# Kernel optimization log

Measured on AMD Instinct MI355X. Metric: run time of the kernel, lower is better.

The kernel has to match this reference:

```python
import jax, jax.numpy as jnp
import numpy as np

BETA = 0.25  # commitment_beta


def setup_inputs() -> dict:
    key = jax.random.key(0)
    k1, k2 = jax.random.split(key)
    B, C, H, W = 8, 256, 32, 32
    n_embed = 16384
    x = jax.random.normal(k1, (B, C, H, W), dtype=jnp.float32)
    # torch init: uniform_(-1/codebook_size, 1/codebook_size)
    weight = jax.random.uniform(k2, (n_embed, C), dtype=jnp.float32,
                                minval=-1.0 / n_embed, maxval=1.0 / n_embed)
    return {"x": x, "weight": weight}


def reference(x, weight):
    B, C, H, W = x.shape
    # b c h w -> b (h w) c
    xf = jnp.transpose(x, (0, 2, 3, 1)).reshape(B, H * W, C)
    flat = xf.reshape(-1, C)  # [N, C], N = B*H*W
    d = (jnp.sum(flat * flat, axis=1, keepdims=True)
         + jnp.sum(weight * weight, axis=1)[None, :]
         - 2.0 * flat @ weight.T)
    idx = jnp.argmin(d, axis=-1)          # [N]
    xq = weight[idx].reshape(B, H * W, C)  # codebook gather
    sg = jax.lax.stop_gradient
    loss = (BETA * jnp.mean((sg(xq) - xf) ** 2)
            + jnp.mean((xq - sg(xf)) ** 2))
    # straight-through estimator
    xq_st = xf + sg(xq - xf)
    # b (h w) c -> b c h w
    xq_img = jnp.transpose(xq_st.reshape(B, H, W, C), (0, 3, 1, 2))
    x_code = idx.reshape(B, H, W)
    return xq_img, loss, x_code
```

## Files before the change

### kernel.cpp

```cpp
#include <hip/hip_runtime.h>
#include <stdint.h>

#define NROW    8192
#define CDIM    256
#define NCODE   16384
#define MARGINF 6.0e-5f

typedef short short8 __attribute__((ext_vector_type(8)));
typedef float floatx4 __attribute__((ext_vector_type(4)));
typedef _Float16 half2v __attribute__((ext_vector_type(2)));

__device__ inline ushort f2bf(float f) {
    unsigned u = __builtin_bit_cast(unsigned, f);
    unsigned r = (u + 0x7fffu + ((u >> 16) & 1u)) >> 16;
    return (ushort)r;
}
__device__ inline unsigned fsort(float v) {
    unsigned u = __builtin_bit_cast(unsigned, v);
    return (u >> 31) ? ~u : (u | 0x80000000u);
}

__device__ inline void gl_lds16(const ushort* g, ushort* lds) {
    __builtin_amdgcn_global_load_lds(
        (const __attribute__((address_space(1))) unsigned int*)(g),
        (__attribute__((address_space(3))) unsigned int*)(lds),
        16, 0, 0);
}

__global__ __launch_bounds__(256) void prep_x(const float* __restrict__ x,
                                              float* __restrict__ xf32,
                                              ushort* __restrict__ xbf) {
    __shared__ float tile[32][33];
    const int b = blockIdx.x, ht = blockIdx.y, ct = blockIdx.z;
    const int t = threadIdx.x;
    const int hw0 = ht * 32, c0 = ct * 32;
    {
        const int cc = t >> 5, hh = t & 31;
        #pragma unroll
        for (int i = 0; i < 4; ++i) {
            int cl = cc + i * 8;
            tile[cl][hh] = x[((size_t)(b * 256 + c0 + cl) << 10) + hw0 + hh];
        }
    }
    __syncthreads();
    {
        const int col = t & 31, row = t >> 5;
        #pragma unroll
        for (int i = 0; i < 4; ++i) {
            int r = row + i * 8;
            float v = tile[col][r];
            size_t o = ((size_t)(b * 1024 + hw0 + r) << 8) + c0 + col;
            xf32[o] = v;
            xbf[o] = f2bf(v);
        }
    }
}

__global__ __launch_bounds__(256) void prep_w2(const float* __restrict__ w,
                                               ushort* __restrict__ wbf,
                                               float* __restrict__ S2a) {
#pragma clang fp contract(off)
    const int gt = blockIdx.x * 256 + threadIdx.x;
    const int j = gt >> 1, h = gt & 1;
    const float* a = w + ((size_t)j << 8) + h * 128;
    ushort* orow = wbf + ((size_t)j << 8) + h * 128;
    float r8[8];
    #pragma unroll
    for (int l = 0; l < 8; ++l) { float v = a[l]; r8[l] = v * v; }
    for (int i = 8; i < 128; i += 8) {
        #pragma unroll
        for (int l = 0; l < 8; ++l) { float v = a[i + l]; r8[l] = r8[l] + v * v; }
    }
    float hs = ((r8[0] + r8[1]) + (r8[2] + r8[3])) + ((r8[4] + r8[5]) + (r8[6] + r8[7]));
    float other = __shfl_xor(hs, 1);
    if (h == 0) S2a[j] = hs + other;
    for (int i = 0; i < 128; i += 8) {
        ushort u8[8];
        #pragma unroll
        for (int l = 0; l < 8; ++l) u8[l] = f2bf(a[i + l]);
        *(ushort4*)(orow + i)     = make_ushort4(u8[0], u8[1], u8[2], u8[3]);
        *(ushort4*)(orow + i + 4) = make_ushort4(u8[4], u8[5], u8[6], u8[7]);
    }
}

__global__ __launch_bounds__(256) void gemm_min(const ushort* __restrict__ Wb,
                                                const ushort* __restrict__ Xb,
                                                const float* __restrict__ S2a,
                                                ushort* __restrict__ bm16) {
    __shared__ __attribute__((aligned(16))) ushort As[8192];
    __shared__ __attribute__((aligned(16))) ushort Bs[8192];
    __shared__ __attribute__((aligned(16))) ushort stg[128 * 8];

    const int n0 = blockIdx.x * 128;
    const int j0 = blockIdx.y * 128;
    const int t  = threadIdx.x;
    const int wv = t >> 6, l = t & 63;
    const int wr = wv >> 1, wc = wv & 1;
    const int q  = l >> 4, c = l & 15;

    const int lr = l >> 3;
    const int lperm = (l & 7) ^ lr;
    const size_t gA0 = ((size_t)(j0 + wv * 32 + lr) << 8) + lperm * 8;
    const size_t gB0 = ((size_t)(n0 + wv * 32 + lr) << 8) + lperm * 8;
    const int ldsbase = wv * 2048;

    floatx4 acc[4][4];
    #pragma unroll
    for (int mi = 0; mi < 4; ++mi)
        #pragma unroll
        for (int ni = 0; ni < 4; ++ni)
            acc[mi][ni] = (floatx4){0.f, 0.f, 0.f, 0.f};

    for (int kb = 0; kb < 4; ++kb) {
        if (kb) __syncthreads();
        #pragma unroll
        for (int ca = 0; ca < 4; ++ca) {
            gl_lds16(Wb + gA0 + ca * 2048 + kb * 64, As + ldsbase + ca * 512);
            gl_lds16(Xb + gB0 + ca * 2048 + kb * 64, Bs + ldsbase + ca * 512);
        }
        __syncthreads();
        #pragma unroll
        for (int kk = 0; kk < 2; ++kk) {
            short8 af[4], bf[4];
            #pragma unroll
            for (int mi = 0; mi < 4; ++mi) {
                int row = wr * 64 + mi * 16 + c;
                int pos = (kk * 4 + q) ^ (c & 7);
                af[mi] = *(const short8*)&As[row * 64 + pos * 8];
            }
            #pragma unroll
            for (int ni = 0; ni < 4; ++ni) {
                int row = wc * 64 + ni * 16 + c;
                int pos = (kk * 4 + q) ^ (c & 7);
                bf[ni] = *(const short8*)&Bs[row * 64 + pos * 8];
            }
            #pragma unroll
            for (int mi = 0; mi < 4; ++mi)
                #pragma unroll
                for (int ni = 0; ni < 4; ++ni)
                    acc[mi][ni] = __builtin_amdgcn_mfma_f32_16x16x32_bf16(
                        af[mi], bf[ni], acc[mi][ni], 0, 0, 0);
        }
    }

    #pragma unroll
    for (int mi = 0; mi < 4; ++mi) {
        float4 s2 = *(const float4*)&S2a[j0 + wr * 64 + mi * 16 + (q << 2)];
        #pragma unroll
        for (int ni = 0; ni < 4; ++ni) {
            float m0 = fmaf(-2.f, acc[mi][ni][0], s2.x);
            float m1 = fmaf(-2.f, acc[mi][ni][1], s2.y);
            float m2 = fmaf(-2.f, acc[mi][ni][2], s2.z);
            float m3 = fmaf(-2.f, acc[mi][ni][3], s2.w);
            float m = fminf(fminf(m0, m1), fminf(m2, m3));
            m = fminf(m, __shfl_xor(m, 16));
            m = fminf(m, __shfl_xor(m, 32));
            if (q == 0) {
                int qr = wc * 64 + ni * 16 + c;
                stg[qr * 8 + wr * 4 + mi] =
                    __builtin_bit_cast(ushort, (_Float16)m);
            }
        }
    }
    __syncthreads();
    if (t < 128) {
        uint4 v = *(const uint4*)&stg[t * 8];
        *(uint4*)(bm16 + ((size_t)(n0 + t) << 10) + blockIdx.y * 8) = v;
    }
}

__global__ __launch_bounds__(256) void rescore5(const ushort* __restrict__ bm16,
                                                const float* __restrict__ xf32,
                                                const float* __restrict__ w,
                                                const float* __restrict__ S2a,
                                                int* __restrict__ idxb,
                                                float* __restrict__ xcode,
                                                float* __restrict__ lpart) {
#pragma clang fp contract(off)
    __shared__ float xs[4][256];
    __shared__ short list[4][128];
    __shared__ int ncand[4];

    const int t = threadIdx.x, wv = t >> 6, l = t & 63;
    const int n = blockIdx.x * 4 + wv;
    if (l == 0) ncand[wv] = 0;

    const float4 xv = *(const float4*)&xf32[((size_t)n << 8) + l * 4];
    *(float4*)&xs[wv][l * 4] = xv;

    const uint4* bp = (const uint4*)(bm16 + ((size_t)n << 10) + l * 16);
    const uint4 b0 = bp[0], b1 = bp[1];
    float vals[16];
    {
        unsigned uu[8] = {b0.x, b0.y, b0.z, b0.w, b1.x, b1.y, b1.z, b1.w};
        #pragma unroll
        for (int i = 0; i < 8; ++i) {
            half2v h = __builtin_bit_cast(half2v, uu[i]);
            vals[2 * i]     = (float)h[0];
            vals[2 * i + 1] = (float)h[1];
        }
    }
    float vmin = vals[0];
    #pragma unroll
    for (int i = 1; i < 16; ++i) vmin = fminf(vmin, vals[i]);
    #pragma unroll
    for (int off = 1; off <= 32; off <<= 1) vmin = fminf(vmin, __shfl_xor(vmin, off));
    const float thr = vmin + MARGINF;
    #pragma unroll
    for (int i = 0; i < 16; ++i)
        if (vals[i] <= thr) {
            int p = atomicAdd(&ncand[wv], 1);
            if (p < 128) list[wv][p] = (short)(l * 16 + i);
        }

    float racc = 0.f;
    if (l < 16) {
        const float* a_ = &xs[wv][(l >> 3) * 128];
        const int ai = l & 7;
        float v = a_[ai];
        racc = v * v;
        for (int i = 8; i < 128; i += 8) { v = a_[i + ai]; racc = racc + v * v; }
    }
    racc = racc + __shfl_xor(racc, 1);
    racc = racc + __shfl_xor(racc, 2);
    racc = racc + __shfl_xor(racc, 4);
    racc = racc + __shfl_xor(racc, 8);
    const float S1n = __shfl(racc, 0);

    const int ntot = (ncand[wv] < 128 ? ncand[wv] : 128) * 16;
    unsigned long long best = ~0ull;
    for (int s = l; s < ntot; s += 64) {
        const int j = (int)list[wv][s >> 4] * 16 + (s & 15);
        const float4* wr4 = (const float4*)(w + ((size_t)j << 8));
        float g = 0.f;
        #pragma unroll
        for (int half = 0; half < 4; ++half) {
            float4 buf[16];
            #pragma unroll
            for (int i = 0; i < 16; ++i) buf[i] = wr4[half * 16 + i];
            #pragma unroll
            for (int i = 0; i < 16; ++i) {
                const float4 xv4 = *(const float4*)&xs[wv][half * 64 + i * 4];
                g = fmaf(xv4.x, buf[i].x, g);
                g = fmaf(xv4.y, buf[i].y, g);
                g = fmaf(xv4.z, buf[i].z, g);
                g = fmaf(xv4.w, buf[i].w, g);
            }
        }
        float d = (S1n + S2a[j]) - 2.0f * g;
        unsigned long long key = ((unsigned long long)fsort(d) << 32) | (unsigned)j;
        if (key < best) best = key;
    }
    #pragma unroll
    for (int off = 1; off <= 32; off <<= 1) {
        unsigned long long o = __shfl_xor(best, off);
        if (o < best) best = o;
    }
    const int J = (int)(best & 0xffffffffu);
    const float4 wj = *(const float4*)&w[((size_t)J << 8) + l * 4];
    float d0 = wj.x - xv.x, d1 = wj.y - xv.y, d2 = wj.z - xv.z, d3 = wj.w - xv.w;
    float lacc = (d0 * d0 + d1 * d1) + (d2 * d2 + d3 * d3);
    #pragma unroll
    for (int off = 1; off <= 32; off <<= 1) lacc += __shfl_xor(lacc, off);
    if (l == 0) {
        idxb[n] = J;
        xcode[n] = (float)J;
        lpart[n] = lacc;
    }
}

__global__ __launch_bounds__(256) void loss_fin(const float* __restrict__ lpart,
                                                float* __restrict__ loss) {
    __shared__ float red[256];
    const int t = threadIdx.x;
    float s = 0.f;
    for (int i = 0; i < 32; ++i) s += lpart[t + (i << 8)];
    red[t] = s;
    __syncthreads();
    for (int k = 128; k > 0; k >>= 1) {
        if (t < k) red[t] += red[t + k];
        __syncthreads();
    }
    if (t == 0) *loss = red[0] * (1.25f / 2097152.0f);
}

__global__ __launch_bounds__(256) void outputs_k(const float* __restrict__ w,
                                                 const int* __restrict__ idxb,
                                                 float* __restrict__ out) {
    const int b = blockIdx.x, hq = blockIdx.y, cs = blockIdx.z;
    const int t = threadIdx.x;
    const int hw = hq * 256 + t;
    const int n = (b << 10) + hw;
    const int id = idxb[n];
    #pragma unroll 4
    for (int ci = 0; ci < 32; ++ci) {
        const int c_ = cs * 32 + ci;
        const size_t oo = ((size_t)((b << 8) + c_) << 10) + hw;
        out[oo] = w[((size_t)id << 8) + c_];
    }
}

extern "C" void kernel_launch(void* const* d_in, const int* in_sizes, int n_in,
                              void* d_out, int out_size, void* d_ws, size_t ws_size,
                              hipStream_t stream) {
    const float* x = (const float*)d_in[0];
    const float* w = (const float*)d_in[1];
    float* out = (float*)d_out;

    char* ws = (char*)d_ws;
    const size_t MB = 1024u * 1024u;
    ushort* xbf   = (ushort*)(ws);
    float*  xf32  = (float*) (ws + 4 * MB);
    ushort* wbf   = (ushort*)(ws + 12 * MB);
    float*  S2a   = (float*) (ws + 20 * MB);
    ushort* bm16  = (ushort*)(ws + 21 * MB);
    int*    idxb  = (int*)   (ws + 37 * MB);
    float*  lpart = (float*) (ws + 37 * MB + 65536);

    float* loss_ptr  = out + 2097152;
    float* xcode_ptr = out + 2097153;

    prep_x  <<<dim3(8, 32, 8), 256, 0, stream>>>(x, xf32, xbf);
    prep_w2 <<<dim3(128),      256, 0, stream>>>(w, wbf, S2a);
    gemm_min<<<dim3(64, 128),  256, 0, stream>>>(wbf, xbf, S2a, bm16);
    rescore5<<<dim3(2048),     256, 0, stream>>>(bm16, xf32, w, S2a, idxb,
                                                 xcode_ptr, lpart);
    loss_fin<<<dim3(1),        256, 0, stream>>>(lpart, loss_ptr);
    outputs_k<<<dim3(8, 4, 8), 256, 0, stream>>>(w, idxb, out);
}
```

Measured before the change: 268.5 us.

## Fuse prep kernels and fold output scatter and loss reduction into rescore

Merges prep_x and prep_w2 into a single launch split by block index. Rescore now writes the gathered codebook row straight into the NCHW output and reduces the loss through a last-block-done atomic counter, which removes the separate loss_fin and outputs_k kernels and the idx buffer. This saves launch overhead and a second pass over the gathered weights. The cost is a strided scatter store from rescore, with each wave writing 256 channels at stride 1024 floats, plus an atomic and threadfence per block.

```diff
diff --git a/kernel.cpp b/kernel.cpp
--- a/kernel.cpp
+++ b/kernel.cpp
@@ -27,59 +27,63 @@
         16, 0, 0);
 }
 
-__global__ __launch_bounds__(256) void prep_x(const float* __restrict__ x,
-                                              float* __restrict__ xf32,
-                                              ushort* __restrict__ xbf) {
-    __shared__ float tile[32][33];
-    const int b = blockIdx.x, ht = blockIdx.y, ct = blockIdx.z;
+__global__ __launch_bounds__(256) void prep_all(const float* __restrict__ x,
+                                                const float* __restrict__ w,
+                                                float* __restrict__ xf32,
+                                                ushort* __restrict__ xbf,
+                                                ushort* __restrict__ wbf,
+                                                float* __restrict__ S2a,
+                                                int* __restrict__ ctr) {
+#pragma clang fp contract(off)
+    const int bid = blockIdx.x;
     const int t = threadIdx.x;
-    const int hw0 = ht * 32, c0 = ct * 32;
-    {
-        const int cc = t >> 5, hh = t & 31;
-        #pragma unroll
-        for (int i = 0; i < 4; ++i) {
-            int cl = cc + i * 8;
-            tile[cl][hh] = x[((size_t)(b * 256 + c0 + cl) << 10) + hw0 + hh];
-        }
-    }
-    __syncthreads();
-    {
-        const int col = t & 31, row = t >> 5;
-        #pragma unroll
-        for (int i = 0; i < 4; ++i) {
-            int r = row + i * 8;
-            float v = tile[col][r];
-            size_t o = ((size_t)(b * 1024 + hw0 + r) << 8) + c0 + col;
-            xf32[o] = v;
-            xbf[o] = f2bf(v);
-        }
-    }
-}
-
-__global__ __launch_bounds__(256) void prep_w2(const float* __restrict__ w,
-                                               ushort* __restrict__ wbf,
-                                               float* __restrict__ S2a) {
-#pragma clang fp contract(off)
-    const int gt = blockIdx.x * 256 + threadIdx.x;
-    const int j = gt >> 1, h = gt & 1;
-    const float* a = w + ((size_t)j << 8) + h * 128;
-    ushort* orow = wbf + ((size_t)j << 8) + h * 128;
-    float r8[8];
-    #pragma unroll
-    for (int l = 0; l < 8; ++l) { float v = a[l]; r8[l] = v * v; }
-    for (int i = 8; i < 128; i += 8) {
-        #pragma unroll
-        for (int l = 0; l < 8; ++l) { float v = a[i + l]; r8[l] = r8[l] + v * v; }
-    }
-    float hs = ((r8[0] + r8[1]) + (r8[2] + r8[3])) + ((r8[4] + r8[5]) + (r8[6] + r8[7]));
-    float other = __shfl_xor(hs, 1);
-    if (h == 0) S2a[j] = hs + other;
-    for (int i = 0; i < 128; i += 8) {
-        ushort u8[8];
-        #pragma unroll
-        for (int l = 0; l < 8; ++l) u8[l] = f2bf(a[i + l]);
-        *(ushort4*)(orow + i)     = make_ushort4(u8[0], u8[1], u8[2], u8[3]);
-        *(ushort4*)(orow + i + 4) = make_ushort4(u8[4], u8[5], u8[6], u8[7]);
+    if (bid < 2048) {
+        __shared__ float tile[32][33];
+        const int b = bid & 7, ht = (bid >> 3) & 31, ct = bid >> 8;
+        const int hw0 = ht * 32, c0 = ct * 32;
+        {
+            const int cc = t >> 5, hh = t & 31;
+            #pragma unroll
+            for (int i = 0; i < 4; ++i) {
+                int cl = cc + i * 8;
+                tile[cl][hh] = x[((size_t)(b * 256 + c0 + cl) << 10) + hw0 + hh];
+            }
+        }
+        __syncthreads();
+        {
+            const int col = t & 31, row = t >> 5;
+            #pragma unroll
+            for (int i = 0; i < 4; ++i) {
+                int r = row + i * 8;
+                float v = tile[col][r];
+                size_t o = ((size_t)(b * 1024 + hw0 + r) << 8) + c0 + col;
+                xf32[o] = v;
+                xbf[o] = f2bf(v);
+            }
+        }
+    } else {
+        if (bid == 2048 && t == 0) *ctr = 0;
+        const int gt = (bid - 2048) * 256 + t;
+        const int j = gt >> 1, h = gt & 1;
+        const float* a = w + ((size_t)j << 8) + h * 128;
+        ushort* orow = wbf + ((size_t)j << 8) + h * 128;
+        float r8[8];
+        #pragma unroll
+        for (int l = 0; l < 8; ++l) { float v = a[l]; r8[l] = v * v; }
+        for (int i = 8; i < 128; i += 8) {
+            #pragma unroll
+            for (int l = 0; l < 8; ++l) { float v = a[i + l]; r8[l] = r8[l] + v * v; }
+        }
+        float hs = ((r8[0] + r8[1]) + (r8[2] + r8[3])) + ((r8[4] + r8[5]) + (r8[6] + r8[7]));
+        float other = __shfl_xor(hs, 1);
+        if (h == 0) S2a[j] = hs + other;
+        for (int i = 0; i < 128; i += 8) {
+            ushort u8[8];
+            #pragma unroll
+            for (int l = 0; l < 8; ++l) u8[l] = f2bf(a[i + l]);
+            *(ushort4*)(orow + i)     = make_ushort4(u8[0], u8[1], u8[2], u8[3]);
+            *(ushort4*)(orow + i + 4) = make_ushort4(u8[4], u8[5], u8[6], u8[7]);
+        }
     }
 }
 
@@ -169,17 +173,21 @@
     }
 }
 
-__global__ __launch_bounds__(256) void rescore5(const ushort* __restrict__ bm16,
+__global__ __launch_bounds__(256) void rescore6(const ushort* __restrict__ bm16,
                                                 const float* __restrict__ xf32,
                                                 const float* __restrict__ w,
                                                 const float* __restrict__ S2a,
-                                                int* __restrict__ idxb,
+                                                float* __restrict__ out,
                                                 float* __restrict__ xcode,
-                                                float* __restrict__ lpart) {
+                                                float* __restrict__ lpart,
+                                                int* __restrict__ ctr,
+                                                float* __restrict__ loss) {
 #pragma clang fp contract(off)
     __shared__ float xs[4][256];
     __shared__ short list[4][128];
     __shared__ int ncand[4];
+    __shared__ float wp[4];
+    __shared__ int is_last;
 
     const int t = threadIdx.x, wv = t >> 6, l = t & 63;
     const int n = blockIdx.x * 4 + wv;
@@ -257,46 +265,41 @@
         if (o < best) best = o;
     }
     const int J = (int)(best & 0xffffffffu);
+    if (l == 0) xcode[n] = (float)J;
+
     const float4 wj = *(const float4*)&w[((size_t)J << 8) + l * 4];
+    {
+        float* ob = out + ((size_t)(n >> 10) << 18) + ((size_t)l << 12) + (n & 1023);
+        ob[0]    = wj.x;
+        ob[1024] = wj.y;
+        ob[2048] = wj.z;
+        ob[3072] = wj.w;
+    }
     float d0 = wj.x - xv.x, d1 = wj.y - xv.y, d2 = wj.z - xv.z, d3 = wj.w - xv.w;
     float lacc = (d0 * d0 + d1 * d1) + (d2 * d2 + d3 * d3);
     #pragma unroll
     for (int off = 1; off <= 32; off <<= 1) lacc += __shfl_xor(lacc, off);
-    if (l == 0) {
-        idxb[n] = J;
-        xcode[n] = (float)J;
-        lpart[n] = lacc;
-    }
-}
-
-__global__ __launch_bounds__(256) void loss_fin(const float* __restrict__ lpart,
-                                                float* __restrict__ loss) {
-    __shared__ float red[256];
-    const int t = threadIdx.x;
-    float s = 0.f;
-    for (int i = 0; i < 32; ++i) s += lpart[t + (i << 8)];
-    red[t] = s;
+    if (l == 0) wp[wv] = lacc;
     __syncthreads();
-    for (int k = 128; k > 0; k >>= 1) {
-        if (t < k) red[t] += red[t + k];
+    if (t == 0) {
+        lpart[blockIdx.x] = (wp[0] + wp[1]) + (wp[2] + wp[3]);
+        __threadfence();
+        int old = atomicAdd(ctr, 1);
+        is_last = (old == (int)gridDim.x - 1) ? 1 : 0;
+    }
+    __syncthreads();
+    if (is_last) {
+        __threadfence();
+        __shared__ float red[256];
+        float s = 0.f;
+        for (int i = t; i < 2048; i += 256) s += lpart[i];
+        red[t] = s;
         __syncthreads();
-    }
-    if (t == 0) *loss = red[0] * (1.25f / 2097152.0f);
-}
-
-__global__ __launch_bounds__(256) void outputs_k(const float* __restrict__ w,
-                                                 const int* __restrict__ idxb,
-                                                 float* __restrict__ out) {
-    const int b = blockIdx.x, hq = blockIdx.y, cs = blockIdx.z;
-    const int t = threadIdx.x;
-    const int hw = hq * 256 + t;
-    const int n = (b << 10) + hw;
-    const int id = idxb[n];
-    #pragma unroll 4
-    for (int ci = 0; ci < 32; ++ci) {
-        const int c_ = cs * 32 + ci;
-        const size_t oo = ((size_t)((b << 8) + c_) << 10) + hw;
-        out[oo] = w[((size_t)id << 8) + c_];
+        for (int k = 128; k > 0; k >>= 1) {
+            if (t < k) red[t] += red[t + k];
+            __syncthreads();
+        }
+        if (t == 0) *loss = red[0] * (1.25f / 2097152.0f);
     }
 }
 
@@ -314,17 +317,14 @@
     ushort* wbf   = (ushort*)(ws + 12 * MB);
     float*  S2a   = (float*) (ws + 20 * MB);
     ushort* bm16  = (ushort*)(ws + 21 * MB);
-    int*    idxb  = (int*)   (ws + 37 * MB);
-    float*  lpart = (float*) (ws + 37 * MB + 65536);
+    float*  lpart = (float*) (ws + 37 * MB);
+    int*    ctr   = (int*)   (ws + 37 * MB + 16384);
 
     float* loss_ptr  = out + 2097152;
     float* xcode_ptr = out + 2097153;
 
-    prep_x  <<<dim3(8, 32, 8), 256, 0, stream>>>(x, xf32, xbf);
-    prep_w2 <<<dim3(128),      256, 0, stream>>>(w, wbf, S2a);
+    prep_all<<<dim3(2176),     256, 0, stream>>>(x, w, xf32, xbf, wbf, S2a, ctr);
     gemm_min<<<dim3(64, 128),  256, 0, stream>>>(wbf, xbf, S2a, bm16);
-    rescore5<<<dim3(2048),     256, 0, stream>>>(bm16, xf32, w, S2a, idxb,
-                                                 xcode_ptr, lpart);
-    loss_fin<<<dim3(1),        256, 0, stream>>>(lpart, loss_ptr);
-    outputs_k<<<dim3(8, 4, 8), 256, 0, stream>>>(w, idxb, out);
-}
+    rescore6<<<dim3(2048),     256, 0, stream>>>(bm16, xf32, w, S2a, out,
+                                                 xcode_ptr, lpart, ctr, loss_ptr);
+}
```

Result: slower. 310.6 us (+15.6%).

## Encode per-block argmin and second-min gap to shrink rescore candidate sets

Applied to the files above, without the earlier changes.

The GEMM epilogue now tracks, for each 16-code group, the minimum, its index and a quantized gap to the second minimum, packed into 32 bits. The rescore kernel uses this to check only the single best code for most candidate groups, and expands a full 16-code group only when the second minimum also falls within the margin. This cuts the exact fp32 rescoring work, at the cost of doubling the size of the block-min buffer and adding epilogue ALU and shuffle work. The two prep kernels are also merged into one launch, and the loss reduction is folded into the outputs kernel, removing two launches.

```diff
diff --git a/kernel.cpp b/kernel.cpp
--- a/kernel.cpp
+++ b/kernel.cpp
@@ -8,7 +8,6 @@
 
 typedef short short8 __attribute__((ext_vector_type(8)));
 typedef float floatx4 __attribute__((ext_vector_type(4)));
-typedef _Float16 half2v __attribute__((ext_vector_type(2)));
 
 __device__ inline ushort f2bf(float f) {
     unsigned u = __builtin_bit_cast(unsigned, f);
@@ -27,69 +26,71 @@
         16, 0, 0);
 }
 
-__global__ __launch_bounds__(256) void prep_x(const float* __restrict__ x,
-                                              float* __restrict__ xf32,
-                                              ushort* __restrict__ xbf) {
-    __shared__ float tile[32][33];
-    const int b = blockIdx.x, ht = blockIdx.y, ct = blockIdx.z;
+__global__ __launch_bounds__(256) void prep_all(const float* __restrict__ x,
+                                                const float* __restrict__ w,
+                                                float* __restrict__ xf32,
+                                                ushort* __restrict__ xbf,
+                                                ushort* __restrict__ wbf,
+                                                float* __restrict__ S2a) {
+#pragma clang fp contract(off)
+    const int bid = blockIdx.x;
     const int t = threadIdx.x;
-    const int hw0 = ht * 32, c0 = ct * 32;
-    {
-        const int cc = t >> 5, hh = t & 31;
-        #pragma unroll
-        for (int i = 0; i < 4; ++i) {
-            int cl = cc + i * 8;
-            tile[cl][hh] = x[((size_t)(b * 256 + c0 + cl) << 10) + hw0 + hh];
-        }
-    }
-    __syncthreads();
-    {
-        const int col = t & 31, row = t >> 5;
-        #pragma unroll
-        for (int i = 0; i < 4; ++i) {
-            int r = row + i * 8;
-            float v = tile[col][r];
-            size_t o = ((size_t)(b * 1024 + hw0 + r) << 8) + c0 + col;
-            xf32[o] = v;
-            xbf[o] = f2bf(v);
-        }
-    }
-}
-
-__global__ __launch_bounds__(256) void prep_w2(const float* __restrict__ w,
-                                               ushort* __restrict__ wbf,
-                                               float* __restrict__ S2a) {
-#pragma clang fp contract(off)
-    const int gt = blockIdx.x * 256 + threadIdx.x;
-    const int j = gt >> 1, h = gt & 1;
-    const float* a = w + ((size_t)j << 8) + h * 128;
-    ushort* orow = wbf + ((size_t)j << 8) + h * 128;
-    float r8[8];
-    #pragma unroll
-    for (int l = 0; l < 8; ++l) { float v = a[l]; r8[l] = v * v; }
-    for (int i = 8; i < 128; i += 8) {
-        #pragma unroll
-        for (int l = 0; l < 8; ++l) { float v = a[i + l]; r8[l] = r8[l] + v * v; }
-    }
-    float hs = ((r8[0] + r8[1]) + (r8[2] + r8[3])) + ((r8[4] + r8[5]) + (r8[6] + r8[7]));
-    float other = __shfl_xor(hs, 1);
-    if (h == 0) S2a[j] = hs + other;
-    for (int i = 0; i < 128; i += 8) {
-        ushort u8[8];
-        #pragma unroll
-        for (int l = 0; l < 8; ++l) u8[l] = f2bf(a[i + l]);
-        *(ushort4*)(orow + i)     = make_ushort4(u8[0], u8[1], u8[2], u8[3]);
-        *(ushort4*)(orow + i + 4) = make_ushort4(u8[4], u8[5], u8[6], u8[7]);
+    if (bid < 2048) {
+        __shared__ float tile[32][33];
+        const int b = bid & 7, ht = (bid >> 3) & 31, ct = bid >> 8;
+        const int hw0 = ht * 32, c0 = ct * 32;
+        {
+            const int cc = t >> 5, hh = t & 31;
+            #pragma unroll
+            for (int i = 0; i < 4; ++i) {
+                int cl = cc + i * 8;
+                tile[cl][hh] = x[((size_t)(b * 256 + c0 + cl) << 10) + hw0 + hh];
+            }
+        }
+        __syncthreads();
+        {
+            const int col = t & 31, row = t >> 5;
+            #pragma unroll
+            for (int i = 0; i < 4; ++i) {
+                int r = row + i * 8;
+                float v = tile[col][r];
+                size_t o = ((size_t)(b * 1024 + hw0 + r) << 8) + c0 + col;
+                xf32[o] = v;
+                xbf[o] = f2bf(v);
+            }
+        }
+    } else {
+        const int gt = (bid - 2048) * 256 + t;
+        const int j = gt >> 1, h = gt & 1;
+        const float* a = w + ((size_t)j << 8) + h * 128;
+        ushort* orow = wbf + ((size_t)j << 8) + h * 128;
+        float r8[8];
+        #pragma unroll
+        for (int l = 0; l < 8; ++l) { float v = a[l]; r8[l] = v * v; }
+        for (int i = 8; i < 128; i += 8) {
+            #pragma unroll
+            for (int l = 0; l < 8; ++l) { float v = a[i + l]; r8[l] = r8[l] + v * v; }
+        }
+        float hs = ((r8[0] + r8[1]) + (r8[2] + r8[3])) + ((r8[4] + r8[5]) + (r8[6] + r8[7]));
+        float other = __shfl_xor(hs, 1);
+        if (h == 0) S2a[j] = hs + other;
+        for (int i = 0; i < 128; i += 8) {
+            ushort u8[8];
+            #pragma unroll
+            for (int l = 0; l < 8; ++l) u8[l] = f2bf(a[i + l]);
+            *(ushort4*)(orow + i)     = make_ushort4(u8[0], u8[1], u8[2], u8[3]);
+            *(ushort4*)(orow + i + 4) = make_ushort4(u8[4], u8[5], u8[6], u8[7]);
+        }
     }
 }
 
 __global__ __launch_bounds__(256) void gemm_min(const ushort* __restrict__ Wb,
                                                 const ushort* __restrict__ Xb,
                                                 const float* __restrict__ S2a,
-                                                ushort* __restrict__ bm16) {
+                                                unsigned* __restrict__ bm32) {
     __shared__ __attribute__((aligned(16))) ushort As[8192];
     __shared__ __attribute__((aligned(16))) ushort Bs[8192];
-    __shared__ __attribute__((aligned(16))) ushort stg[128 * 8];
+    __shared__ __attribute__((aligned(16))) unsigned stg32[128][8];
 
     const int n0 = blockIdx.x * 128;
     const int j0 = blockIdx.y * 128;
@@ -148,28 +149,50 @@
         float4 s2 = *(const float4*)&S2a[j0 + wr * 64 + mi * 16 + (q << 2)];
         #pragma unroll
         for (int ni = 0; ni < 4; ++ni) {
-            float m0 = fmaf(-2.f, acc[mi][ni][0], s2.x);
-            float m1 = fmaf(-2.f, acc[mi][ni][1], s2.y);
-            float m2 = fmaf(-2.f, acc[mi][ni][2], s2.z);
-            float m3 = fmaf(-2.f, acc[mi][ni][3], s2.w);
-            float m = fminf(fminf(m0, m1), fminf(m2, m3));
-            m = fminf(m, __shfl_xor(m, 16));
-            m = fminf(m, __shfl_xor(m, 32));
+            float v0 = fmaf(-2.f, acc[mi][ni][0], s2.x);
+            float v1 = fmaf(-2.f, acc[mi][ni][1], s2.y);
+            float v2 = fmaf(-2.f, acc[mi][ni][2], s2.z);
+            float v3 = fmaf(-2.f, acc[mi][ni][3], s2.w);
+            float lo01 = fminf(v0, v1), hi01 = fmaxf(v0, v1);
+            float lo23 = fminf(v2, v3), hi23 = fmaxf(v2, v3);
+            int   i01 = v1 < v0 ? 1 : 0;
+            int   i23 = v3 < v2 ? 3 : 2;
+            float m1 = fminf(lo01, lo23);
+            float m2 = fminf(fmaxf(lo01, lo23), lo23 < lo01 ? hi23 : hi01);
+            int   i1 = (q << 2) | (lo23 < lo01 ? i23 : i01);
+            #pragma unroll
+            for (int off = 16; off <= 32; off <<= 1) {
+                float om1 = __shfl_xor(m1, off);
+                float om2 = __shfl_xor(m2, off);
+                int   oi1 = __shfl_xor(i1, off);
+                float nm2 = fminf(fminf(m2, om2), fmaxf(m1, om1));
+                i1 = om1 < m1 ? oi1 : i1;
+                m1 = fminf(m1, om1);
+                m2 = nm2;
+            }
             if (q == 0) {
-                int qr = wc * 64 + ni * 16 + c;
-                stg[qr * 8 + wr * 4 + mi] =
-                    __builtin_bit_cast(ushort, (_Float16)m);
+                ushort min16 = __builtin_bit_cast(ushort, (_Float16)m1);
+                float delta = m2 - m1;
+                ushort d16 = __builtin_bit_cast(ushort, (_Float16)delta);
+                ushort d8 = d16 >> 8;
+                float rec = (float)__builtin_bit_cast(_Float16, (ushort)(d8 << 8));
+                if (rec > delta && d8) d8--;
+                stg32[wc * 64 + ni * 16 + c][wr * 4 + mi] =
+                    ((unsigned)min16 << 16) | ((unsigned)d8 << 8) | (unsigned)i1;
             }
         }
     }
     __syncthreads();
     if (t < 128) {
-        uint4 v = *(const uint4*)&stg[t * 8];
-        *(uint4*)(bm16 + ((size_t)(n0 + t) << 10) + blockIdx.y * 8) = v;
-    }
-}
-
-__global__ __launch_bounds__(256) void rescore5(const ushort* __restrict__ bm16,
+        uint4 a0 = *(const uint4*)&stg32[t][0];
+        uint4 a1 = *(const uint4*)&stg32[t][4];
+        size_t base = ((size_t)(n0 + t) << 10) + blockIdx.y * 8;
+        *(uint4*)(bm32 + base)     = a0;
+        *(uint4*)(bm32 + base + 4) = a1;
+    }
+}
+
+__global__ __launch_bounds__(256) void rescore7(const unsigned* __restrict__ bm32,
                                                 const float* __restrict__ xf32,
                                                 const float* __restrict__ w,
                                                 const float* __restrict__ S2a,
@@ -178,28 +201,33 @@
                                                 float* __restrict__ lpart) {
 #pragma clang fp contract(off)
     __shared__ float xs[4][256];
-    __shared__ short list[4][128];
-    __shared__ int ncand[4];
+    __shared__ short sing[4][128];
+    __shared__ short blk[4][32];
+    __shared__ int ns[4], nb[4];
 
     const int t = threadIdx.x, wv = t >> 6, l = t & 63;
     const int n = blockIdx.x * 4 + wv;
-    if (l == 0) ncand[wv] = 0;
+    if (l == 0) { ns[wv] = 0; nb[wv] = 0; }
 
     const float4 xv = *(const float4*)&xf32[((size_t)n << 8) + l * 4];
     *(float4*)&xs[wv][l * 4] = xv;
 
-    const uint4* bp = (const uint4*)(bm16 + ((size_t)n << 10) + l * 16);
-    const uint4 b0 = bp[0], b1 = bp[1];
+    const unsigned* bp = bm32 + ((size_t)n << 10) + l * 16;
+    unsigned ee[16];
+    {
+        uint4 e0 = *(const uint4*)(bp);
+        uint4 e1 = *(const uint4*)(bp + 4);
+        uint4 e2 = *(const uint4*)(bp + 8);
+        uint4 e3 = *(const uint4*)(bp + 12);
+        ee[0]=e0.x; ee[1]=e0.y; ee[2]=e0.z; ee[3]=e0.w;
+        ee[4]=e1.x; ee[5]=e1.y; ee[6]=e1.z; ee[7]=e1.w;
+        ee[8]=e2.x; ee[9]=e2.y; ee[10]=e2.z; ee[11]=e2.w;
+        ee[12]=e3.x; ee[13]=e3.y; ee[14]=e3.z; ee[15]=e3.w;
+    }
     float vals[16];
-    {
-        unsigned uu[8] = {b0.x, b0.y, b0.z, b0.w, b1.x, b1.y, b1.z, b1.w};
-        #pragma unroll
-        for (int i = 0; i < 8; ++i) {
-            half2v h = __builtin_bit_cast(half2v, uu[i]);
-            vals[2 * i]     = (float)h[0];
-            vals[2 * i + 1] = (float)h[1];
-        }
-    }
+    #pragma unroll
+    for (int i = 0; i < 16; ++i)
+        vals[i] = (float)__builtin_bit_cast(_Float16, (ushort)(ee[i] >> 16));
     float vmin = vals[0];
     #pragma unroll
     for (int i = 1; i < 16; ++i) vmin = fminf(vmin, vals[i]);
@@ -207,11 +235,19 @@
     for (int off = 1; off <= 32; off <<= 1) vmin = fminf(vmin, __shfl_xor(vmin, off));
     const float thr = vmin + MARGINF;
     #pragma unroll
-    for (int i = 0; i < 16; ++i)
+    for (int i = 0; i < 16; ++i) {
         if (vals[i] <= thr) {
-            int p = atomicAdd(&ncand[wv], 1);
-            if (p < 128) list[wv][p] = (short)(l * 16 + i);
-        }
+            const int jb = l * 16 + i;
+            int p = atomicAdd(&ns[wv], 1);
+            if (p < 128) sing[wv][p] = (short)(jb * 16 + (int)(ee[i] & 15u));
+            float dr = (float)__builtin_bit_cast(_Float16,
+                           (ushort)(((ee[i] >> 8) & 0xFFu) << 8));
+            if (vals[i] + dr <= thr) {
+                int pb = atomicAdd(&nb[wv], 1);
+                if (pb < 32) blk[wv][pb] = (short)jb;
+            }
+        }
+    }
 
     float racc = 0.f;
     if (l < 16) {
@@ -227,10 +263,14 @@
     racc = racc + __shfl_xor(racc, 8);
     const float S1n = __shfl(racc, 0);
 
-    const int ntot = (ncand[wv] < 128 ? ncand[wv] : 128) * 16;
+    const int nsv = ns[wv] < 128 ? ns[wv] : 128;
+    const int nbv = nb[wv] < 32 ? nb[wv] : 32;
+    const int ntot = nsv + nbv * 16;
     unsigned long long best = ~0ull;
     for (int s = l; s < ntot; s += 64) {
-        const int j = (int)list[wv][s >> 4] * 16 + (s & 15);
+        const int j = (s < nsv)
+            ? (int)sing[wv][s]
+            : (int)blk[wv][(s - nsv) >> 4] * 16 + ((s - nsv) & 15);
         const float4* wr4 = (const float4*)(w + ((size_t)j << 8));
         float g = 0.f;
         #pragma unroll
@@ -257,6 +297,7 @@
         if (o < best) best = o;
     }
     const int J = (int)(best & 0xffffffffu);
+
     const float4 wj = *(const float4*)&w[((size_t)J << 8) + l * 4];
     float d0 = wj.x - xv.x, d1 = wj.y - xv.y, d2 = wj.z - xv.z, d3 = wj.w - xv.w;
     float lacc = (d0 * d0 + d1 * d1) + (d2 * d2 + d3 * d3);
@@ -269,24 +310,11 @@
     }
 }
 
-__global__ __launch_bounds__(256) void loss_fin(const float* __restrict__ lpart,
-                                                float* __restrict__ loss) {
-    __shared__ float red[256];
-    const int t = threadIdx.x;
-    float s = 0.f;
-    for (int i = 0; i < 32; ++i) s += lpart[t + (i << 8)];
-    red[t] = s;
-    __syncthreads();
-    for (int k = 128; k > 0; k >>= 1) {
-        if (t < k) red[t] += red[t + k];
-        __syncthreads();
-    }
-    if (t == 0) *loss = red[0] * (1.25f / 2097152.0f);
-}
-
 __global__ __launch_bounds__(256) void outputs_k(const float* __restrict__ w,
                                                  const int* __restrict__ idxb,
-                                                 float* __restrict__ out) {
+                                                 const float* __restrict__ lpart,
+                                                 float* __restrict__ out,
+                                                 float* __restrict__ loss) {
     const int b = blockIdx.x, hq = blockIdx.y, cs = blockIdx.z;
     const int t = threadIdx.x;
     const int hw = hq * 256 + t;
@@ -298,6 +326,18 @@
         const size_t oo = ((size_t)((b << 8) + c_) << 10) + hw;
         out[oo] = w[((size_t)id << 8) + c_];
     }
+    if (b == 0 && hq == 0 && cs == 0) {
+        __shared__ float red[256];
+        float s = 0.f;
+        for (int i = 0; i < 32; ++i) s += lpart[t + (i << 8)];
+        red[t] = s;
+        __syncthreads();
+        for (int k = 128; k > 0; k >>= 1) {
+            if (t < k) red[t] += red[t + k];
+            __syncthreads();
+        }
+        if (t == 0) *loss = red[0] * (1.25f / 2097152.0f);
+    }
 }
 
 extern "C" void kernel_launch(void* const* d_in, const int* in_sizes, int n_in,
@@ -309,22 +349,20 @@
 
     char* ws = (char*)d_ws;
     const size_t MB = 1024u * 1024u;
-    ushort* xbf   = (ushort*)(ws);
-    float*  xf32  = (float*) (ws + 4 * MB);
-    ushort* wbf   = (ushort*)(ws + 12 * MB);
-    float*  S2a   = (float*) (ws + 20 * MB);
-    ushort* bm16  = (ushort*)(ws + 21 * MB);
-    int*    idxb  = (int*)   (ws + 37 * MB);
-    float*  lpart = (float*) (ws + 37 * MB + 65536);
+    ushort*   xbf   = (ushort*)  (ws);
+    float*    xf32  = (float*)   (ws + 4 * MB);
+    ushort*   wbf   = (ushort*)  (ws + 12 * MB);
+    float*    S2a   = (float*)   (ws + 20 * MB);
+    unsigned* bm32  = (unsigned*)(ws + 21 * MB);
+    int*      idxb  = (int*)     (ws + 53 * MB);
+    float*    lpart = (float*)   (ws + 53 * MB + 65536);
 
     float* loss_ptr  = out + 2097152;
     float* xcode_ptr = out + 2097153;
 
-    prep_x  <<<dim3(8, 32, 8), 256, 0, stream>>>(x, xf32, xbf);
-    prep_w2 <<<dim3(128),      256, 0, stream>>>(w, wbf, S2a);
-    gemm_min<<<dim3(64, 128),  256, 0, stream>>>(wbf, xbf, S2a, bm16);
-    rescore5<<<dim3(2048),     256, 0, stream>>>(bm16, xf32, w, S2a, idxb,
+    prep_all<<<dim3(2176),     256, 0, stream>>>(x, w, xf32, xbf, wbf, S2a);
+    gemm_min<<<dim3(64, 128),  256, 0, stream>>>(wbf, xbf, S2a, bm32);
+    rescore7<<<dim3(2048),     256, 0, stream>>>(bm32, xf32, w, S2a, idxb,
                                                  xcode_ptr, lpart);
-    loss_fin<<<dim3(1),        256, 0, stream>>>(lpart, loss_ptr);
-    outputs_k<<<dim3(8, 4, 8), 256, 0, stream>>>(w, idxb, out);
-}
+    outputs_k<<<dim3(8, 4, 8), 256, 0, stream>>>(w, idxb, lpart, out, loss_ptr);
+}
```

Result: slower. 286.4 us (+6.7%).
